# Kernel tuning notes

Measured on AMD Instinct MI355X. Metric: run time of the kernel, lower is better.

The kernel has to match this reference:

```python
import jax, jax.numpy as jnp
import numpy as np
from jax import lax

L = 4          # num_layers
DIM = 1024
HEADS = 4
DH = DIM // HEADS
MLP_H = 4 * DIM
EPS = 1e-5
SCALE = 1.0 / (DIM ** 0.5)  # note: module scales by 1/sqrt(dim), not 1/sqrt(head_dim)


def layer_norm(x, g, b):
    mu = jnp.mean(x, axis=-1, keepdims=True)
    var = jnp.var(x, axis=-1, keepdims=True)
    return (x - mu) * jax.lax.rsqrt(var + EPS) * g + b


def setup_inputs() -> dict:
    key = jax.random.key(0)
    ks = jax.random.split(key, 12)
    s = 0.02
    img = jax.random.normal(ks[0], (2, 2, 16, 192, 192), dtype=jnp.float32)
    conv_w = jax.random.normal(ks[1], (DIM, 2, 2, 8, 8), dtype=jnp.float32) * s
    conv_b = jnp.zeros((DIM,), jnp.float32)
    n_tokens = 24 * 24 * 8
    pos = jax.random.normal(ks[2], (1, n_tokens, DIM), dtype=jnp.float32) * s
    ln1_g = jnp.ones((L, DIM), jnp.float32); ln1_b = jnp.zeros((L, DIM), jnp.float32)
    ln2_g = jnp.ones((L, DIM), jnp.float32); ln2_b = jnp.zeros((L, DIM), jnp.float32)
    qkv_w = jax.random.normal(ks[3], (L, DIM, 3 * DIM), dtype=jnp.float32) * s
    out_w = jax.random.normal(ks[4], (L, DIM, DIM), dtype=jnp.float32) * s
    out_b = jnp.zeros((L, DIM), jnp.float32)
    fc1_w = jax.random.normal(ks[5], (L, DIM, MLP_H), dtype=jnp.float32) * s
    fc1_b = jnp.zeros((L, MLP_H), jnp.float32)
    fc2_w = jax.random.normal(ks[6], (L, MLP_H, DIM), dtype=jnp.float32) * s
    fc2_b = jnp.zeros((L, DIM), jnp.float32)
    lnf_g = jnp.ones((DIM,), jnp.float32); lnf_b = jnp.zeros((DIM,), jnp.float32)
    return dict(img=img, conv_w=conv_w, conv_b=conv_b, pos=pos,
                ln1_g=ln1_g, ln1_b=ln1_b, qkv_w=qkv_w, out_w=out_w, out_b=out_b,
                ln2_g=ln2_g, ln2_b=ln2_b, fc1_w=fc1_w, fc1_b=fc1_b,
                fc2_w=fc2_w, fc2_b=fc2_b, lnf_g=lnf_g, lnf_b=lnf_b)


def reference(img, conv_w, conv_b, pos, ln1_g, ln1_b, qkv_w, out_w, out_b,
              ln2_g, ln2_b, fc1_w, fc1_b, fc2_w, fc2_b, lnf_g, lnf_b):
    # Patch embed: Conv3d stride==kernel, NCDHW
    p = lax.conv_general_dilated(img, conv_w, window_strides=(2, 8, 8),
                                 padding='VALID',
                                 dimension_numbers=('NCDHW', 'OIDHW', 'NCDHW'))
    p = p + conv_b[None, :, None, None, None]
    b = p.shape[0]
    x = p.reshape(b, DIM, -1).transpose(0, 2, 1)  # (b, n, dim), n = D*H*W order
    x = x + pos

    for i in range(L):
        x1 = layer_norm(x, ln1_g[i], ln1_b[i])
        n = x1.shape[1]
        qkv = (x1 @ qkv_w[i]).reshape(b, n, 3, HEADS, DH)
        q, k, v = (qkv[:, :, j].transpose(0, 2, 1, 3) for j in range(3))  # (b,h,n,dh)
        dot = jnp.einsum('bhnd,bhmd->bhnm', q, k) * SCALE
        attn = jax.nn.softmax(dot, axis=-1)
        o = jnp.einsum('bhnm,bhmd->bhnd', attn, v)
        o = o.transpose(0, 2, 1, 3).reshape(b, n, DIM)
        x = x + (o @ out_w[i] + out_b[i])

        x2 = layer_norm(x, ln2_g[i], ln2_b[i])
        h = jax.nn.gelu(x2 @ fc1_w[i] + fc1_b[i], approximate=False)
        x = x + (h @ fc2_w[i] + fc2_b[i])

    return layer_norm(x, lnf_g, lnf_b)
```

## Files before the change

### kernel.cpp

```cpp
#include <hip/hip_runtime.h>


typedef unsigned short u16;
typedef __bf16 bf16v8 __attribute__((ext_vector_type(8)));
typedef float f32v4 __attribute__((ext_vector_type(4)));
typedef float f32x16 __attribute__((ext_vector_type(16)));

#define NTOK   4608
#define TTOT   9216
#define DIMD   1024
#define H3     3072
#define MLPH   4096
#define NHEAD  4
#define DHEAD  256
#define NLAYER 4
#define KVB    64
#define NKT    (NTOK / KVB)

__device__ __forceinline__ u16 f2bf(float f) {
  unsigned u = __float_as_uint(f);
  u += 0x7fffu + ((u >> 16) & 1u);
  return (u16)(u >> 16);
}
__device__ __forceinline__ float bf2f(u16 b) {
  return __uint_as_float(((unsigned)b) << 16);
}
__device__ __forceinline__ void gload16(const void* g, void* l) {
  __builtin_amdgcn_global_load_lds((__attribute__((address_space(1))) void*)g,
                                   (__attribute__((address_space(3))) void*)l,
                                   16, 0, 0);
}

__global__ __launch_bounds__(256) void transpose_w(
    const float* __restrict__ src, u16* __restrict__ dst, int R, int C) {
  __shared__ float tile[32][33];
  const int c0 = blockIdx.x * 32, r0 = blockIdx.y * 32;
  const int tx = threadIdx.x, ty = threadIdx.y;
#pragma unroll
  for (int i = 0; i < 32; i += 8)
    tile[ty + i][tx] = src[(size_t)(r0 + ty + i) * C + c0 + tx];
  __syncthreads();
#pragma unroll
  for (int i = 0; i < 32; i += 8)
    dst[(size_t)(c0 + ty + i) * R + r0 + tx] = f2bf(tile[tx][ty + i]);
}

__global__ __launch_bounds__(256) void convert_bf16(
    const float* __restrict__ src, u16* __restrict__ dst, int n) {
  int i = blockIdx.x * 256 + threadIdx.x;
  if (i < n) dst[i] = f2bf(src[i]);
}

__global__ __launch_bounds__(256) void patch_extract(
    const float* __restrict__ img, u16* __restrict__ A) {
  const int t = blockIdx.x;
  const int k = threadIdx.x;
  const int b = t / NTOK, r = t % NTOK;
  const int d = r / 576, r2 = r % 576;
  const int hh = r2 / 24, ww = r2 % 24;
  const int ci = k >> 7, k2 = k & 127;
  const int kd = k2 >> 6, k3 = k2 & 63;
  const int kh = k3 >> 3, kw = k3 & 7;
  const size_t idx =
      ((size_t)((b * 2 + ci) * 16 + (2 * d + kd))) * (192 * 192) +
      (size_t)(8 * hh + kh) * 192 + (8 * ww + kw);
  A[(size_t)t * 256 + k] = f2bf(img[idx]);
}

template <int OUTF32>
__global__ __launch_bounds__(256) void ln_kernel(
    const float* __restrict__ x, const float* __restrict__ g,
    const float* __restrict__ bta, void* __restrict__ out) {
  const size_t row = blockIdx.x;
  const int t = threadIdx.x;
  const float4 v = ((const float4*)(x + row * DIMD))[t];
  float s = v.x + v.y + v.z + v.w;
  float ss = v.x * v.x + v.y * v.y + v.z * v.z + v.w * v.w;
#pragma unroll
  for (int o = 32; o; o >>= 1) {
    s += __shfl_xor(s, o, 64);
    ss += __shfl_xor(ss, o, 64);
  }
  __shared__ float sh[8];
  if ((t & 63) == 0) { sh[t >> 6] = s; sh[4 + (t >> 6)] = ss; }
  __syncthreads();
  s = sh[0] + sh[1] + sh[2] + sh[3];
  ss = sh[4] + sh[5] + sh[6] + sh[7];
  const float mu = s * (1.f / DIMD);
  const float rs = rsqrtf(ss * (1.f / DIMD) - mu * mu + 1e-5f);
  const float4 gg = ((const float4*)g)[t];
  const float4 bb = ((const float4*)bta)[t];
  const float y0 = (v.x - mu) * rs * gg.x + bb.x;
  const float y1 = (v.y - mu) * rs * gg.y + bb.y;
  const float y2 = (v.z - mu) * rs * gg.z + bb.z;
  const float y3 = (v.w - mu) * rs * gg.w + bb.w;
  if (OUTF32) {
    float4 o4; o4.x = y0; o4.y = y1; o4.z = y2; o4.w = y3;
    ((float4*)out)[row * 256 + t] = o4;
  } else {
    ushort4 o4;
    o4.x = f2bf(y0); o4.y = f2bf(y1); o4.z = f2bf(y2); o4.w = f2bf(y3);
    ((ushort4*)out)[row * 256 + t] = o4;
  }
}

__global__ __launch_bounds__(256) void transpose_v(
    const u16* __restrict__ qkv, u16* __restrict__ vT) {
  const int bh = blockIdx.z, b = bh >> 2, h = bh & 3;
  const u16* src = qkv + (size_t)b * NTOK * H3 + 2048 + h * DHEAD;
  u16* dst = vT + (size_t)bh * DHEAD * NTOK;
  __shared__ u16 tile[32][33];
  const int t0 = blockIdx.x * 32, d0 = blockIdx.y * 32;
  const int tx = threadIdx.x, ty = threadIdx.y;
#pragma unroll
  for (int i = 0; i < 32; i += 8)
    tile[ty + i][tx] = src[(size_t)(t0 + ty + i) * H3 + d0 + tx];
  __syncthreads();
#pragma unroll
  for (int i = 0; i < 32; i += 8)
    dst[(size_t)(d0 + ty + i) * NTOK + t0 + tx] = tile[tx][ty + i];
}

__global__ __launch_bounds__(512, 2) void flash_attn(
    const u16* __restrict__ qkv, const u16* __restrict__ vT,
    u16* __restrict__ obuf) {
  __shared__ __align__(16) u16 Ks[2][KVB * 256];
  __shared__ __align__(16) u16 Vs[2][256 * KVB];

  const int tid = threadIdx.x;
  const int lane = tid & 63, w = tid >> 6;
  const int c = lane & 31, h32 = lane >> 5;
  const int bh = blockIdx.x & 7, b = bh >> 2, h = bh & 3;
  const int t0 = (blockIdx.x >> 3) * 256;

  const u16* qkv_b = qkv + (size_t)b * NTOK * H3;
  const u16* vt_bh = vT + (size_t)bh * (size_t)DHEAD * NTOK;
  const int kcol = DIMD + h * DHEAD;
  const int csw = (c & 7) << 4;

  bf16v8 qf[16];
  {
    const u16* qrow = qkv_b + (size_t)(t0 + w * 32 + c) * H3 + h * DHEAD + h32 * 8;
#pragma unroll
    for (int ks = 0; ks < 16; ks++)
      qf[ks] = *reinterpret_cast<const bf16v8*>(qrow + ks * 16);
  }

  f32x16 o[8];
#pragma unroll
  for (int dt = 0; dt < 8; dt++)
#pragma unroll
    for (int r = 0; r < 16; r++) o[dt][r] = 0.f;
  float m = -1e30f, l = 0.f;

  auto stage = [&](int kt) {
    const int buf = kt & 1;
    const int kt0 = kt * KVB;
#pragma unroll
    for (int i = 0; i < 4; i++) {
      const int q = i * 512 + tid;
      const int row = q >> 5;
      const int sb = ((q & 31) * 16) ^ ((row & 7) << 4);
      gload16(qkv_b + (size_t)(kt0 + row) * H3 + kcol + (sb >> 1),
              (char*)&Ks[buf][0] + (size_t)q * 16);
    }
#pragma unroll
    for (int i = 0; i < 4; i++) {
      const int q = i * 512 + tid;
      const int r = q >> 3;
      const int sb = ((q & 7) * 16) ^ ((r & 7) << 4);
      gload16(vt_bh + (size_t)r * NTOK + kt0 + (sb >> 1),
              (char*)&Vs[buf][0] + (size_t)q * 16);
    }
  };

  stage(0);

  for (int kt = 0; kt < NKT; kt++) {
    __syncthreads();
    if (kt + 1 < NKT) stage(kt + 1);

    const char* kb = (const char*)&Ks[kt & 1][0];
    const char* vb = (const char*)&Vs[kt & 1][0];

#pragma unroll
    for (int tt = 0; tt < 2; tt++) {
      f32x16 st;
#pragma unroll
      for (int r = 0; r < 16; r++) st[r] = 0.f;
      const char* krow = kb + (tt * 32 + c) * 512;
#pragma unroll
      for (int ks = 0; ks < 16; ks++) {
        const bf16v8 kf =
            *reinterpret_cast<const bf16v8*>(krow + ((ks * 32 + h32 * 16) ^ csw));
        st = __builtin_amdgcn_mfma_f32_32x32x16_bf16(kf, qf[ks], st, 0, 0, 0);
      }

      float mx = st[0];
#pragma unroll
      for (int r = 1; r < 16; r++) mx = fmaxf(mx, st[r]);
      mx = fmaxf(mx, __shfl_xor(mx, 32, 64));
      const float pm = mx * 0.03125f;
      if (__any(pm > m + 8.f)) {
        const float mn = fmaxf(m, pm);
        const float corr = __expf(m - mn);
        m = mn; l *= corr;
#pragma unroll
        for (int dt = 0; dt < 8; dt++)
#pragma unroll
          for (int r = 0; r < 16; r++) o[dt][r] *= corr;
      }
      float sum = 0.f;
#pragma unroll
      for (int r = 0; r < 16; r++) {
        const float p = __expf(st[r] * 0.03125f - m);
        st[r] = p; sum += p;
      }
      sum += __shfl_xor(sum, 32, 64);
      l += sum;

#pragma unroll
      for (int g = 0; g < 2; g++) {
        const int rb = g * 8;
        float z[4];
#pragma unroll
        for (int k = 0; k < 4; k++) {
          const float y = h32 ? st[rb + k] : st[rb + 4 + k];
          z[k] = __shfl_xor(y, 32, 64);
        }
        union { u16 u[8]; bf16v8 v; } pb;
#pragma unroll
        for (int k = 0; k < 4; k++) {
          pb.u[k]     = f2bf(h32 ? z[k] : st[rb + k]);
          pb.u[4 + k] = f2bf(h32 ? st[rb + 4 + k] : z[k]);
        }
        const int s = tt * 2 + g;
#pragma unroll
        for (int dt = 0; dt < 8; dt++) {
          const bf16v8 vf = *reinterpret_cast<const bf16v8*>(
              vb + (dt * 32 + c) * 128 + ((s * 32 + h32 * 16) ^ csw));
          o[dt] = __builtin_amdgcn_mfma_f32_32x32x16_bf16(vf, pb.v, o[dt], 0, 0, 0);
        }
      }
    }
  }

  const float rl = 1.f / l;
  u16* orow = obuf + (size_t)(b * NTOK + t0 + w * 32 + c) * DIMD + h * DHEAD;
#pragma unroll
  for (int dt = 0; dt < 8; dt++) {
#pragma unroll
    for (int rq = 0; rq < 4; rq++) {
      ushort4 v4;
      v4.x = f2bf(o[dt][rq * 4 + 0] * rl);
      v4.y = f2bf(o[dt][rq * 4 + 1] * rl);
      v4.z = f2bf(o[dt][rq * 4 + 2] * rl);
      v4.w = f2bf(o[dt][rq * 4 + 3] * rl);
      *reinterpret_cast<ushort4*>(orow + dt * 32 + rq * 8 + h32 * 4) = v4;
    }
  }
}

template <int EPI>
__global__ __launch_bounds__(256) void gemm_bt(
    const u16* __restrict__ A, int lda,
    const u16* __restrict__ Bt, int ldb,
    int K, void* __restrict__ Cp, int ldc,
    const float* __restrict__ bias, const float* __restrict__ extra,
    float scale) {
  __shared__ __align__(16) u16 As[128 * 32];
  __shared__ __align__(16) u16 Bs[128 * 32];
  const int tid = threadIdx.x;
  const int bm = blockIdx.x, bn = blockIdx.y;

  const int c0 = tid, c1 = tid + 256;
  const u16* Ab = A + (size_t)(bm * 128) * lda;
  const u16* Bb = Bt + (size_t)(bn * 128) * ldb;
  const size_t a0 = (size_t)(c0 >> 2) * lda + (c0 & 3) * 8;
  const size_t a1 = (size_t)(c1 >> 2) * lda + (c1 & 3) * 8;
  const size_t b0 = (size_t)(c0 >> 2) * ldb + (c0 & 3) * 8;
  const size_t b1 = (size_t)(c1 >> 2) * ldb + (c1 & 3) * 8;

  const int lane = tid & 63;
  const int wv = tid >> 6;
  const int wm = (wv >> 1) * 64;
  const int wn = (wv & 1) * 64;
  const int fr = lane & 15;
  const int fk = (lane >> 4) * 8;

  f32v4 acc[4][4];
#pragma unroll
  for (int m = 0; m < 4; m++)
#pragma unroll
    for (int n = 0; n < 4; n++) acc[m][n] = (f32v4){0.f, 0.f, 0.f, 0.f};

  for (int k0 = 0; k0 < K; k0 += 32) {
    __syncthreads();
    gload16(Ab + a0 + k0, As + (size_t)c0 * 8);
    gload16(Ab + a1 + k0, As + (size_t)c1 * 8);
    gload16(Bb + b0 + k0, Bs + (size_t)c0 * 8);
    gload16(Bb + b1 + k0, Bs + (size_t)c1 * 8);
    __syncthreads();

    bf16v8 af[4], bq[4];
#pragma unroll
    for (int m = 0; m < 4; m++)
      af[m] = *reinterpret_cast<const bf16v8*>(&As[(wm + m * 16 + fr) * 32 + fk]);
#pragma unroll
    for (int n = 0; n < 4; n++)
      bq[n] = *reinterpret_cast<const bf16v8*>(&Bs[(wn + n * 16 + fr) * 32 + fk]);
#pragma unroll
    for (int m = 0; m < 4; m++)
#pragma unroll
      for (int n = 0; n < 4; n++)
        acc[m][n] =
            __builtin_amdgcn_mfma_f32_16x16x32_bf16(af[m], bq[n], acc[m][n], 0, 0, 0);
  }

  const int rbase = bm * 128 + wm + (lane >> 4) * 4;
  const int cbase = bn * 128 + wn + fr;
#pragma unroll
  for (int m = 0; m < 4; m++) {
#pragma unroll
    for (int n = 0; n < 4; n++) {
      const int col = cbase + n * 16;
#pragma unroll
      for (int j = 0; j < 4; j++) {
        const int rowi = rbase + m * 16 + j;
        const float v = acc[m][n][j];
        if (EPI == 0) {
          ((u16*)Cp)[(size_t)rowi * ldc + col] = f2bf(v);
        } else if (EPI == 2) {
          float* p = (float*)Cp + (size_t)rowi * ldc + col;
          *p += v + bias[col];
        } else if (EPI == 3) {
          float t = v + bias[col];
          t = 0.5f * t * (1.f + erff(t * 0.70710678118654752f));
          ((u16*)Cp)[(size_t)rowi * ldc + col] = f2bf(t);
        } else {
          ((float*)Cp)[(size_t)rowi * ldc + col] =
              v + bias[col] + extra[(size_t)(rowi % NTOK) * DIMD + col];
        }
      }
    }
  }
}

#define SZ_QKVT ((size_t)H3 * DIMD * 2)
#define SZ_OUTT ((size_t)DIMD * DIMD * 2)
#define SZ_FC1T ((size_t)MLPH * DIMD * 2)
#define SZ_FC2T ((size_t)DIMD * MLPH * 2)
#define SZ_CONVW ((size_t)DIMD * 256 * 2)
#define SZ_X ((size_t)TTOT * DIMD * 4)
#define SZ_XO ((size_t)TTOT * DIMD * 2)
#define SZ_BIGA ((size_t)TTOT * H3 * 2 + (size_t)8 * DHEAD * NTOK * 2)

#define OFF_QKVT ((size_t)0)
#define OFF_OUTT (OFF_QKVT + SZ_QKVT)
#define OFF_FC1T (OFF_OUTT + SZ_OUTT)
#define OFF_FC2T (OFF_FC1T + SZ_FC1T)
#define OFF_CONVW (OFF_FC2T + SZ_FC2T)
#define OFF_X (OFF_CONVW + SZ_CONVW)
#define OFF_XO (OFF_X + SZ_X)
#define OFF_BIGA (OFF_XO + SZ_XO)
#define WS_NEED (OFF_BIGA + SZ_BIGA)

extern "C" void kernel_launch(void* const* d_in, const int* in_sizes, int n_in,
                              void* d_out, int out_size, void* d_ws, size_t ws_size,
                              hipStream_t stream) {
  const float* img = (const float*)d_in[0];
  const float* conv_w = (const float*)d_in[1];
  const float* conv_b = (const float*)d_in[2];
  const float* pos = (const float*)d_in[3];
  const float* ln1_g = (const float*)d_in[4];
  const float* ln1_b = (const float*)d_in[5];
  const float* qkv_w = (const float*)d_in[6];
  const float* out_w = (const float*)d_in[7];
  const float* out_b = (const float*)d_in[8];
  const float* ln2_g = (const float*)d_in[9];
  const float* ln2_b = (const float*)d_in[10];
  const float* fc1_w = (const float*)d_in[11];
  const float* fc1_b = (const float*)d_in[12];
  const float* fc2_w = (const float*)d_in[13];
  const float* fc2_b = (const float*)d_in[14];
  const float* lnf_g = (const float*)d_in[15];
  const float* lnf_b = (const float*)d_in[16];
  float* out = (float*)d_out;

  if (ws_size < WS_NEED) return;

  char* ws = (char*)d_ws;
  u16* qkvT = (u16*)(ws + OFF_QKVT);
  u16* outT = (u16*)(ws + OFF_OUTT);
  u16* fc1T = (u16*)(ws + OFF_FC1T);
  u16* fc2T = (u16*)(ws + OFF_FC2T);
  u16* convW = (u16*)(ws + OFF_CONVW);
  float* x = (float*)(ws + OFF_X);
  u16* x1 = (u16*)(ws + OFF_XO);
  u16* obuf = (u16*)(ws + OFF_XO);
  u16* qkv = (u16*)(ws + OFF_BIGA);
  u16* vT = (u16*)(ws + OFF_BIGA + (size_t)TTOT * H3 * 2);
  u16* hbuf = (u16*)(ws + OFF_BIGA);
  u16* patchA = (u16*)(ws + OFF_BIGA);

  const dim3 tb(32, 8);

  convert_bf16<<<1024, 256, 0, stream>>>(conv_w, convW, DIMD * 256);
  patch_extract<<<TTOT, 256, 0, stream>>>(img, patchA);
  gemm_bt<4><<<dim3(TTOT / 128, DIMD / 128, 1), 256, 0, stream>>>(
      patchA, 256, convW, 256, 256, x, DIMD, conv_b, pos, 1.f);

  for (int l = 0; l < NLAYER; l++) {
    transpose_w<<<dim3(H3 / 32, DIMD / 32, 1), tb, 0, stream>>>(
        qkv_w + (size_t)l * DIMD * H3, qkvT, DIMD, H3);
    transpose_w<<<dim3(DIMD / 32, DIMD / 32, 1), tb, 0, stream>>>(
        out_w + (size_t)l * DIMD * DIMD, outT, DIMD, DIMD);
    transpose_w<<<dim3(MLPH / 32, DIMD / 32, 1), tb, 0, stream>>>(
        fc1_w + (size_t)l * DIMD * MLPH, fc1T, DIMD, MLPH);
    transpose_w<<<dim3(DIMD / 32, MLPH / 32, 1), tb, 0, stream>>>(
        fc2_w + (size_t)l * MLPH * DIMD, fc2T, MLPH, DIMD);

    ln_kernel<0><<<TTOT, 256, 0, stream>>>(x, ln1_g + l * DIMD, ln1_b + l * DIMD, x1);
    gemm_bt<0><<<dim3(TTOT / 128, H3 / 128, 1), 256, 0, stream>>>(
        x1, DIMD, qkvT, DIMD, DIMD, qkv, H3, nullptr, nullptr, 1.f);
    transpose_v<<<dim3(NTOK / 32, DHEAD / 32, 8), tb, 0, stream>>>(qkv, vT);

    flash_attn<<<dim3(18 * 8, 1, 1), 512, 0, stream>>>(qkv, vT, obuf);

    gemm_bt<2><<<dim3(TTOT / 128, DIMD / 128, 1), 256, 0, stream>>>(
        obuf, DIMD, outT, DIMD, DIMD, x, DIMD, out_b + l * DIMD, nullptr, 1.f);
    ln_kernel<0><<<TTOT, 256, 0, stream>>>(x, ln2_g + l * DIMD, ln2_b + l * DIMD, x1);
    gemm_bt<3><<<dim3(TTOT / 128, MLPH / 128, 1), 256, 0, stream>>>(
        x1, DIMD, fc1T, DIMD, DIMD, hbuf, MLPH, fc1_b + l * MLPH, nullptr, 1.f);
    gemm_bt<2><<<dim3(TTOT / 128, DIMD / 128, 1), 256, 0, stream>>>(
        hbuf, MLPH, fc2T, MLPH, MLPH, x, DIMD, fc2_b + l * DIMD, nullptr, 1.f);
  }

  ln_kernel<1><<<TTOT, 256, 0, stream>>>(x, lnf_g, lnf_b, out);
}
```

Baseline: 3.501 ms.

## Halve KV tile and replicate K/V tiles in LDS to cut bank conflicts

Shrinks the attention KV block from 64 to 32 tokens. Each stage now writes two copies of the K and V tiles into LDS, each with a different XOR swizzle phase, and lanes pick a copy by (c>>3)&1 so reads are spread across banks. V is repacked into a 128x64 layout per copy. The change also adds s_setprio around the MFMA loops. The cost is twice as many loop iterations and barriers, plus duplicated global-to-LDS traffic per tile.

```diff
diff --git a/kernel.cpp b/kernel.cpp
--- a/kernel.cpp
+++ b/kernel.cpp
@@ -14,7 +14,7 @@
 #define NHEAD  4
 #define DHEAD  256
 #define NLAYER 4
-#define KVB    64
+#define KVB    32
 #define NKT    (NTOK / KVB)
 
 __device__ __forceinline__ u16 f2bf(float f) {
@@ -124,8 +124,8 @@
 __global__ __launch_bounds__(512, 2) void flash_attn(
     const u16* __restrict__ qkv, const u16* __restrict__ vT,
     u16* __restrict__ obuf) {
-  __shared__ __align__(16) u16 Ks[2][KVB * 256];
-  __shared__ __align__(16) u16 Vs[2][256 * KVB];
+  __shared__ __align__(16) u16 Ks[2][2][KVB * 256];
+  __shared__ __align__(16) u16 Vs[2][2][128 * 64];
 
   const int tid = threadIdx.x;
   const int lane = tid & 63, w = tid >> 6;
@@ -136,7 +136,8 @@
   const u16* qkv_b = qkv + (size_t)b * NTOK * H3;
   const u16* vt_bh = vT + (size_t)bh * (size_t)DHEAD * NTOK;
   const int kcol = DIMD + h * DHEAD;
-  const int csw = (c & 7) << 4;
+  const int rep = (c >> 3) & 1;
+  const int csw = (((c & 7) ^ (rep << 2)) << 4);
 
   bf16v8 qf[16];
   {
@@ -157,20 +158,25 @@
     const int buf = kt & 1;
     const int kt0 = kt * KVB;
 #pragma unroll
-    for (int i = 0; i < 4; i++) {
-      const int q = i * 512 + tid;
-      const int row = q >> 5;
-      const int sb = ((q & 31) * 16) ^ ((row & 7) << 4);
-      gload16(qkv_b + (size_t)(kt0 + row) * H3 + kcol + (sb >> 1),
-              (char*)&Ks[buf][0] + (size_t)q * 16);
-    }
-#pragma unroll
-    for (int i = 0; i < 4; i++) {
-      const int q = i * 512 + tid;
-      const int r = q >> 3;
-      const int sb = ((q & 7) * 16) ^ ((r & 7) << 4);
-      gload16(vt_bh + (size_t)r * NTOK + kt0 + (sb >> 1),
-              (char*)&Vs[buf][0] + (size_t)q * 16);
+    for (int rp = 0; rp < 2; rp++) {
+      const int ph = rp << 2;
+#pragma unroll
+      for (int i = 0; i < 2; i++) {
+        const int q = i * 512 + tid;
+        const int row = q >> 5;
+        const int cb = ((q & 31) * 16) ^ ((((row & 7) ^ ph)) << 4);
+        gload16(qkv_b + (size_t)(kt0 + row) * H3 + kcol + (cb >> 1),
+                (char*)&Ks[buf][rp][0] + (size_t)q * 16);
+      }
+#pragma unroll
+      for (int i = 0; i < 2; i++) {
+        const int q = i * 512 + tid;
+        const int rr = q >> 3;
+        const int p = ((q & 7) * 16) ^ ((((rr & 7) ^ ph)) << 4);
+        const int d = rr + ((p >> 6) << 7);
+        gload16(vt_bh + (size_t)d * NTOK + kt0 + ((p & 63) >> 1),
+                (char*)&Vs[buf][rp][0] + (size_t)q * 16);
+      }
     }
   };
 
@@ -180,68 +186,69 @@
     __syncthreads();
     if (kt + 1 < NKT) stage(kt + 1);
 
-    const char* kb = (const char*)&Ks[kt & 1][0];
-    const char* vb = (const char*)&Vs[kt & 1][0];
-
-#pragma unroll
-    for (int tt = 0; tt < 2; tt++) {
-      f32x16 st;
-#pragma unroll
-      for (int r = 0; r < 16; r++) st[r] = 0.f;
-      const char* krow = kb + (tt * 32 + c) * 512;
-#pragma unroll
-      for (int ks = 0; ks < 16; ks++) {
-        const bf16v8 kf =
-            *reinterpret_cast<const bf16v8*>(krow + ((ks * 32 + h32 * 16) ^ csw));
-        st = __builtin_amdgcn_mfma_f32_32x32x16_bf16(kf, qf[ks], st, 0, 0, 0);
-      }
-
-      float mx = st[0];
-#pragma unroll
-      for (int r = 1; r < 16; r++) mx = fmaxf(mx, st[r]);
-      mx = fmaxf(mx, __shfl_xor(mx, 32, 64));
-      const float pm = mx * 0.03125f;
-      if (__any(pm > m + 8.f)) {
-        const float mn = fmaxf(m, pm);
-        const float corr = __expf(m - mn);
-        m = mn; l *= corr;
-#pragma unroll
-        for (int dt = 0; dt < 8; dt++)
-#pragma unroll
-          for (int r = 0; r < 16; r++) o[dt][r] *= corr;
-      }
-      float sum = 0.f;
-#pragma unroll
-      for (int r = 0; r < 16; r++) {
-        const float p = __expf(st[r] * 0.03125f - m);
-        st[r] = p; sum += p;
-      }
-      sum += __shfl_xor(sum, 32, 64);
-      l += sum;
-
-#pragma unroll
-      for (int g = 0; g < 2; g++) {
-        const int rb = g * 8;
-        float z[4];
-#pragma unroll
-        for (int k = 0; k < 4; k++) {
-          const float y = h32 ? st[rb + k] : st[rb + 4 + k];
-          z[k] = __shfl_xor(y, 32, 64);
-        }
-        union { u16 u[8]; bf16v8 v; } pb;
-#pragma unroll
-        for (int k = 0; k < 4; k++) {
-          pb.u[k]     = f2bf(h32 ? z[k] : st[rb + k]);
-          pb.u[4 + k] = f2bf(h32 ? st[rb + 4 + k] : z[k]);
-        }
-        const int s = tt * 2 + g;
-#pragma unroll
-        for (int dt = 0; dt < 8; dt++) {
-          const bf16v8 vf = *reinterpret_cast<const bf16v8*>(
-              vb + (dt * 32 + c) * 128 + ((s * 32 + h32 * 16) ^ csw));
-          o[dt] = __builtin_amdgcn_mfma_f32_32x32x16_bf16(vf, pb.v, o[dt], 0, 0, 0);
-        }
-      }
+    const char* kb = (const char*)&Ks[kt & 1][rep][0];
+    const char* vb = (const char*)&Vs[kt & 1][rep][0];
+
+    f32x16 st;
+#pragma unroll
+    for (int r = 0; r < 16; r++) st[r] = 0.f;
+    const char* krow = kb + c * 512;
+    __builtin_amdgcn_s_setprio(1);
+#pragma unroll
+    for (int ks = 0; ks < 16; ks++) {
+      const bf16v8 kf =
+          *reinterpret_cast<const bf16v8*>(krow + ((ks * 32 + h32 * 16) ^ csw));
+      st = __builtin_amdgcn_mfma_f32_32x32x16_bf16(kf, qf[ks], st, 0, 0, 0);
+    }
+    __builtin_amdgcn_s_setprio(0);
+
+    float mx = st[0];
+#pragma unroll
+    for (int r = 1; r < 16; r++) mx = fmaxf(mx, st[r]);
+    mx = fmaxf(mx, __shfl_xor(mx, 32, 64));
+    const float pm = mx * 0.03125f;
+    if (__any(pm > m + 8.f)) {
+      const float mn = fmaxf(m, pm);
+      const float corr = __expf(m - mn);
+      m = mn; l *= corr;
+#pragma unroll
+      for (int dt = 0; dt < 8; dt++)
+#pragma unroll
+        for (int r = 0; r < 16; r++) o[dt][r] *= corr;
+    }
+    float sum = 0.f;
+#pragma unroll
+    for (int r = 0; r < 16; r++) {
+      const float p = __expf(st[r] * 0.03125f - m);
+      st[r] = p; sum += p;
+    }
+    sum += __shfl_xor(sum, 32, 64);
+    l += sum;
+
+#pragma unroll
+    for (int s = 0; s < 2; s++) {
+      const int rb = s * 8;
+      float z[4];
+#pragma unroll
+      for (int k = 0; k < 4; k++) {
+        const float y = h32 ? st[rb + k] : st[rb + 4 + k];
+        z[k] = __shfl_xor(y, 32, 64);
+      }
+      union { u16 u[8]; bf16v8 v; } pb;
+#pragma unroll
+      for (int k = 0; k < 4; k++) {
+        pb.u[k]     = f2bf(h32 ? z[k] : st[rb + k]);
+        pb.u[4 + k] = f2bf(h32 ? st[rb + 4 + k] : z[k]);
+      }
+      __builtin_amdgcn_s_setprio(1);
+#pragma unroll
+      for (int dt = 0; dt < 8; dt++) {
+        const int rr = (dt & 3) * 32 + c;
+        const int byte = (((dt >> 2) * 64 + s * 32 + h32 * 16)) ^ csw;
+        const bf16v8 vf = *reinterpret_cast<const bf16v8*>(vb + rr * 128 + byte);
+        o[dt] = __builtin_amdgcn_mfma_f32_32x32x16_bf16(vf, pb.v, o[dt], 0, 0, 0);
+      }
+      __builtin_amdgcn_s_setprio(0);
     }
   }
 
```

Result: faster. 3.242 ms (-7.4%).
